# Optimization experiments

Measured on AMD Instinct MI355X. Metric: run time of the kernel, lower is better.

The kernel has to match this reference:

```python
import jax, jax.numpy as jnp
import numpy as np

N_NODES = 100000
N_EDGES = 1000000
HIDDEN = 64
IN_DIM = 4


def setup_inputs() -> dict:
    key = jax.random.key(0)
    ks = jax.random.split(key, 7)
    x = jax.random.normal(ks[0], (N_NODES, IN_DIM), dtype=jnp.float32)
    edges = jax.random.randint(ks[1], (N_EDGES, 2), 0, N_NODES, dtype=jnp.int32)
    W1 = jax.random.normal(ks[2], (IN_DIM, HIDDEN), dtype=jnp.float32) * 0.5
    b1 = jax.random.normal(ks[3], (HIDDEN,), dtype=jnp.float32) * 0.1
    phases = jax.random.normal(ks[4], (N_EDGES,), dtype=jnp.float32) * 0.1
    Wout = jax.random.normal(ks[5], (HIDDEN, 1), dtype=jnp.float32) * 0.1
    bout = jax.random.normal(ks[6], (1,), dtype=jnp.float32) * 0.1
    return {"x": x, "edges": edges, "W1": W1, "b1": b1,
            "phases": phases, "Wout": Wout, "bout": bout}


def reference(x, edges, W1, b1, phases, Wout, bout):
    # h = lin(x): [N, D]
    h = x @ W1 + b1
    u = edges[:, 0]  # [E]
    v = edges[:, 1]  # [E]
    c = jnp.cos(phases)  # [E]
    s = jnp.sin(phases)  # [E]
    hu = h[u]  # [E, D] gather
    hv = h[v]  # [E, D] gather
    # rot only mixes the first two channels; the rest pass through (eye).
    # msg to v: rot @ h[u] -> [c*h0 - s*h1, s*h0 + c*h1, h2, ...]
    msg_v = jnp.concatenate([
        (c * hu[:, 0] - s * hu[:, 1])[:, None],
        (s * hu[:, 0] + c * hu[:, 1])[:, None],
        hu[:, 2:],
    ], axis=1)
    # msg to u: rot.T @ h[v] -> [c*h0 + s*h1, -s*h0 + c*h1, h2, ...]
    msg_u = jnp.concatenate([
        (c * hv[:, 0] + s * hv[:, 1])[:, None],
        (-s * hv[:, 0] + c * hv[:, 1])[:, None],
        hv[:, 2:],
    ], axis=1)
    diffused = jnp.zeros_like(h).at[v].add(msg_v).at[u].add(msg_u)  # scatter-add
    return (h + diffused) @ Wout + bout  # [N, 1]
```

## Files before the change

kernel.cpp:

```cpp
#include <hip/hip_runtime.h>
#include <hip/hip_fp16.h>

#define N_NODES 100000
#define N_EDGES 1000000
#define HIDDEN 64

#define N_RANGES 3
#define C_RANGE 33344
#define N_SLICES 85
#define PAIRS (N_EDGES / 2)
#define PPB ((PAIRS + N_SLICES - 1) / N_SLICES)
#define A_THREADS 1024

__device__ __forceinline__ void compute_consts(
    const float* __restrict__ W1, const float* __restrict__ b1,
    const float* __restrict__ Wout, const float* __restrict__ bout,
    float* kc, int tid) {
    if (tid < 64) {
        float wj = Wout[tid];
        float p0 = W1[0 * HIDDEN + tid] * wj;
        float p1 = W1[1 * HIDDEN + tid] * wj;
        float p2 = W1[2 * HIDDEN + tid] * wj;
        float p3 = W1[3 * HIDDEN + tid] * wj;
        float pb = b1[tid] * wj;
        #pragma unroll
        for (int off = 32; off > 0; off >>= 1) {
            p0 += __shfl_down(p0, off);
            p1 += __shfl_down(p1, off);
            p2 += __shfl_down(p2, off);
            p3 += __shfl_down(p3, off);
            pb += __shfl_down(pb, off);
        }
        if (tid < 4) {
            kc[5 + tid] = W1[tid * HIDDEN + 0];
            kc[9 + tid] = W1[tid * HIDDEN + 1];
        }
        if (tid == 0) {
            kc[0] = p0; kc[1] = p1; kc[2] = p2; kc[3] = p3; kc[4] = pb;
            kc[13] = b1[0]; kc[14] = b1[1];
            kc[15] = Wout[0]; kc[16] = Wout[1];
            kc[17] = bout[0];
        }
    }
}

__device__ __forceinline__ float contrib(
    float4 xe, float cs, float sn_signed,
    float c0, float c1, float c2, float c3, float cb,
    float a0, float a1, float a2, float a3,
    float g0, float g1, float g2, float g3,
    float b10, float b11, float w0, float w1) {
    float h0 = xe.x * a0 + xe.y * a1 + xe.z * a2 + xe.w * a3 + b10;
    float h1 = xe.x * g0 + xe.y * g1 + xe.z * g2 + xe.w * g3 + b11;
    float d  = xe.x * c0 + xe.y * c1 + xe.z * c2 + xe.w * c3 + cb;
    float a  = h0 * w0 + h1 * w1;
    float b  = h0 * w1 - h1 * w0;
    return cs * a + sn_signed * b + (d - a);
}

__device__ __forceinline__ unsigned pack_half2(float x, float y) {
    __half2 h = __floats2half2_rn(x, y);
    return *(unsigned*)&h;
}

__global__ __launch_bounds__(A_THREADS) void range_kernel(
    const int2* __restrict__ edges, const float* __restrict__ phases,
    const float4* __restrict__ x4,
    const float* __restrict__ W1, const float* __restrict__ b1,
    const float* __restrict__ Wout, const float* __restrict__ bout,
    __half* __restrict__ part) {
    __shared__ float bins[C_RANGE];
    __shared__ float kc[18];
    const int tid = threadIdx.x;
    const int r = blockIdx.x / N_SLICES;
    const int s = blockIdx.x % N_SLICES;

    compute_consts(W1, b1, Wout, bout, kc, tid);
    {
        float4 z = make_float4(0.f, 0.f, 0.f, 0.f);
        float4* b4 = (float4*)bins;
        for (int j = tid; j < C_RANGE / 4; j += A_THREADS) b4[j] = z;
    }
    __syncthreads();

    const float c0 = kc[0], c1 = kc[1], c2 = kc[2], c3 = kc[3], cb = kc[4];
    const float a0 = kc[5], a1 = kc[6], a2 = kc[7], a3 = kc[8];
    const float g0 = kc[9], g1 = kc[10], g2 = kc[11], g3 = kc[12];
    const float b10 = kc[13], b11 = kc[14], w0 = kc[15], w1 = kc[16];

    const int nlo = r * C_RANGE;
    const int pA = s * PPB;
    const int pB = min(pA + PPB, PAIRS);
    const int4*   __restrict__ epairs = (const int4*)edges;
    const float2* __restrict__ ppairs = (const float2*)phases;

    #pragma unroll 2
    for (int p = pA + tid; p < pB; p += A_THREADS) {
        int4   ee = epairs[p];
        float2 pp = ppairs[p];

        unsigned jv0 = (unsigned)(ee.y - nlo);
        unsigned ju0 = (unsigned)(ee.x - nlo);
        unsigned jv1 = (unsigned)(ee.w - nlo);
        unsigned ju1 = (unsigned)(ee.z - nlo);
        bool pv0 = jv0 < C_RANGE, pu0 = ju0 < C_RANGE;
        bool pv1 = jv1 < C_RANGE, pu1 = ju1 < C_RANGE;

        float4 xsv0 = x4[pv0 ? ee.x : 0];
        float4 xsu0 = x4[pu0 ? ee.y : 0];
        float4 xsv1 = x4[pv1 ? ee.z : 0];
        float4 xsu1 = x4[pu1 ? ee.w : 0];

        float sn0, cs0, sn1, cs1;
        __sincosf(pp.x, &sn0, &cs0);
        __sincosf(pp.y, &sn1, &cs1);

        float tv0 = contrib(xsv0, cs0,  sn0, c0,c1,c2,c3,cb, a0,a1,a2,a3, g0,g1,g2,g3, b10,b11,w0,w1);
        float tu0 = contrib(xsu0, cs0, -sn0, c0,c1,c2,c3,cb, a0,a1,a2,a3, g0,g1,g2,g3, b10,b11,w0,w1);
        float tv1 = contrib(xsv1, cs1,  sn1, c0,c1,c2,c3,cb, a0,a1,a2,a3, g0,g1,g2,g3, b10,b11,w0,w1);
        float tu1 = contrib(xsu1, cs1, -sn1, c0,c1,c2,c3,cb, a0,a1,a2,a3, g0,g1,g2,g3, b10,b11,w0,w1);

        if (pv0) atomicAdd(&bins[jv0], tv0);
        if (pu0) atomicAdd(&bins[ju0], tu0);
        if (pv1) atomicAdd(&bins[jv1], tv1);
        if (pu1) atomicAdd(&bins[ju1], tu1);
    }
    __syncthreads();

    uint2* __restrict__ d2 = (uint2*)(part + (size_t)blockIdx.x * C_RANGE);
    const float4* b4 = (const float4*)bins;
    for (int j = tid; j < C_RANGE / 4; j += A_THREADS) {
        float4 v = b4[j];
        d2[j] = make_uint2(pack_half2(v.x, v.y), pack_half2(v.z, v.w));
    }
}

__global__ __launch_bounds__(512) void reduce_kernel(
    const float4* __restrict__ x4,
    const float* __restrict__ W1, const float* __restrict__ b1,
    const float* __restrict__ Wout, const float* __restrict__ bout,
    const __half* __restrict__ part, float* __restrict__ out) {
    __shared__ float kc[18];
    compute_consts(W1, b1, Wout, bout, kc, threadIdx.x);
    __syncthreads();
    int i = blockIdx.x * 512 + threadIdx.x;
    if (i >= N_NODES) return;
    int r = i / C_RANGE;
    int j = i - r * C_RANGE;
    const __half* __restrict__ p = part + ((size_t)(r * N_SLICES)) * C_RANGE + j;
    float sum = 0.0f;
    #pragma unroll 5
    for (int s = 0; s < N_SLICES; s++) sum += __half2float(p[(size_t)s * C_RANGE]);
    float4 xi = x4[i];
    out[i] = sum + xi.x * kc[0] + xi.y * kc[1] + xi.z * kc[2] + xi.w * kc[3]
           + kc[4] + kc[17];
}

__global__ void precompute_kernel(const float* __restrict__ W1,
                                  const float* __restrict__ b1,
                                  const float* __restrict__ Wout,
                                  const float* __restrict__ bout,
                                  float* __restrict__ consts) {
    __shared__ float kc[18];
    compute_consts(W1, b1, Wout, bout, kc, threadIdx.x);
    __syncthreads();
    if (threadIdx.x < 18) consts[threadIdx.x] = kc[threadIdx.x];
}

__global__ void edge_atomic_kernel(const int2* __restrict__ edges,
                                   const float* __restrict__ phases,
                                   const float4* __restrict__ x4,
                                   const float* __restrict__ consts,
                                   float* __restrict__ rep) {
    int e = blockIdx.x * blockDim.x + threadIdx.x;
    if (e >= N_EDGES) return;
    float c0 = consts[0], c1 = consts[1], c2 = consts[2], c3 = consts[3];
    float cb = consts[4];
    float a0 = consts[5], a1 = consts[6], a2 = consts[7], a3 = consts[8];
    float g0 = consts[9], g1 = consts[10], g2 = consts[11], g3 = consts[12];
    float b10 = consts[13], b11 = consts[14], w0 = consts[15], w1 = consts[16];
    int2 ed = edges[e];
    float ph = phases[e];
    float sn, cs;
    __sincosf(ph, &sn, &cs);
    float4 xu = x4[ed.x];
    float4 xv = x4[ed.y];
    atomicAdd(rep + ed.y, contrib(xu, cs,  sn, c0,c1,c2,c3,cb, a0,a1,a2,a3, g0,g1,g2,g3, b10,b11,w0,w1));
    atomicAdd(rep + ed.x, contrib(xv, cs, -sn, c0,c1,c2,c3,cb, a0,a1,a2,a3, g0,g1,g2,g3, b10,b11,w0,w1));
}

__global__ void final_kernel(const float4* __restrict__ x4,
                             const float* __restrict__ consts,
                             const float* __restrict__ rep,
                             float* __restrict__ out) {
    int i = blockIdx.x * blockDim.x + threadIdx.x;
    if (i >= N_NODES) return;
    float4 xi = x4[i];
    out[i] = rep[i] + xi.x * consts[0] + xi.y * consts[1] + xi.z * consts[2]
           + xi.w * consts[3] + consts[4] + consts[17];
}

extern "C" void kernel_launch(void* const* d_in, const int* in_sizes, int n_in,
                              void* d_out, int out_size, void* d_ws, size_t ws_size,
                              hipStream_t stream) {
    const float* x      = (const float*)d_in[0];
    const int*   edges  = (const int*)d_in[1];
    const float* W1     = (const float*)d_in[2];
    const float* b1     = (const float*)d_in[3];
    const float* phases = (const float*)d_in[4];
    const float* Wout   = (const float*)d_in[5];
    const float* bout   = (const float*)d_in[6];
    float* out = (float*)d_out;

    const size_t part_bytes =
        (size_t)N_RANGES * N_SLICES * C_RANGE * sizeof(__half);

    if (ws_size >= part_bytes) {
        __half* part = (__half*)d_ws;
        range_kernel<<<N_RANGES * N_SLICES, A_THREADS, 0, stream>>>(
            (const int2*)edges, phases, (const float4*)x,
            W1, b1, Wout, bout, part);
        reduce_kernel<<<(N_NODES + 511) / 512, 512, 0, stream>>>(
            (const float4*)x, W1, b1, Wout, bout, part, out);
    } else {
        float* consts = (float*)d_ws;
        float* rep    = (float*)((char*)d_ws + 256);
        hipMemsetAsync(rep, 0, N_NODES * sizeof(float), stream);
        precompute_kernel<<<1, 64, 0, stream>>>(W1, b1, Wout, bout, consts);
        edge_atomic_kernel<<<(N_EDGES + 255) / 256, 256, 0, stream>>>(
            (const int2*)edges, phases, (const float4*)x, consts, rep);
        final_kernel<<<(N_NODES + 255) / 256, 256, 0, stream>>>(
            (const float4*)x, consts, rep, out);
    }
}
```

Before: 98.78 us.

## Precompute per-node table, use two ranges with LDS bins plus global overflow atomics

Adds a prep kernel that computes a per-node float4 (a, b, d-a) once, so the edge kernel does two FMAs per message instead of recomputing the linear projection from x. Node ranges drop from 3 to 2 of 50000 nodes, each with 40704 LDS bins and 128 edge slices. Nodes that do not fit in LDS fall back to global atomics on an overflow array. This reads the edge list twice instead of three times and cuts per-edge ALU work, at the cost of global atomic traffic for the overflow nodes, an extra kernel launch and more partial-sum data to reduce.

```diff
diff --git a/kernel.cpp b/kernel.cpp
--- a/kernel.cpp
+++ b/kernel.cpp
@@ -5,9 +5,10 @@
 #define N_EDGES 1000000
 #define HIDDEN 64
 
-#define N_RANGES 3
-#define C_RANGE 33344
-#define N_SLICES 85
+#define N_RANGES 2
+#define R_SPAN   50000
+#define LDS_BINS 40704
+#define N_SLICES 128
 #define PAIRS (N_EDGES / 2)
 #define PPB ((PAIRS + N_SLICES - 1) / N_SLICES)
 #define A_THREADS 1024
@@ -63,36 +64,45 @@
     return *(unsigned*)&h;
 }
 
-__global__ __launch_bounds__(A_THREADS) void range_kernel(
-    const int2* __restrict__ edges, const float* __restrict__ phases,
+__global__ __launch_bounds__(512) void prep_kernel(
     const float4* __restrict__ x4,
     const float* __restrict__ W1, const float* __restrict__ b1,
     const float* __restrict__ Wout, const float* __restrict__ bout,
-    __half* __restrict__ part) {
-    __shared__ float bins[C_RANGE];
+    float4* __restrict__ tab, float* __restrict__ ov) {
     __shared__ float kc[18];
+    compute_consts(W1, b1, Wout, bout, kc, threadIdx.x);
+    __syncthreads();
+    int i = blockIdx.x * 512 + threadIdx.x;
+    if (i >= N_NODES) return;
+    float4 xi = x4[i];
+    float h0 = xi.x * kc[5] + xi.y * kc[6]  + xi.z * kc[7]  + xi.w * kc[8]  + kc[13];
+    float h1 = xi.x * kc[9] + xi.y * kc[10] + xi.z * kc[11] + xi.w * kc[12] + kc[14];
+    float d  = xi.x * kc[0] + xi.y * kc[1]  + xi.z * kc[2]  + xi.w * kc[3]  + kc[4];
+    float a  = h0 * kc[15] + h1 * kc[16];
+    float b  = h0 * kc[16] - h1 * kc[15];
+    tab[i] = make_float4(a, b, d - a, 0.f);
+    ov[i]  = 0.f;
+}
+
+__global__ __launch_bounds__(A_THREADS) void range_kernel(
+    const int4* __restrict__ epairs, const float2* __restrict__ ppairs,
+    const float4* __restrict__ tab,
+    float* __restrict__ ov, __half* __restrict__ part) {
+    __shared__ float bins[LDS_BINS];
     const int tid = threadIdx.x;
-    const int r = blockIdx.x / N_SLICES;
-    const int s = blockIdx.x % N_SLICES;
-
-    compute_consts(W1, b1, Wout, bout, kc, tid);
+    const int r = blockIdx.x >> 7;
+    const int s = blockIdx.x & 127;
+
     {
         float4 z = make_float4(0.f, 0.f, 0.f, 0.f);
         float4* b4 = (float4*)bins;
-        for (int j = tid; j < C_RANGE / 4; j += A_THREADS) b4[j] = z;
-    }
-    __syncthreads();
-
-    const float c0 = kc[0], c1 = kc[1], c2 = kc[2], c3 = kc[3], cb = kc[4];
-    const float a0 = kc[5], a1 = kc[6], a2 = kc[7], a3 = kc[8];
-    const float g0 = kc[9], g1 = kc[10], g2 = kc[11], g3 = kc[12];
-    const float b10 = kc[13], b11 = kc[14], w0 = kc[15], w1 = kc[16];
-
-    const int nlo = r * C_RANGE;
+        for (int j = tid; j < LDS_BINS / 4; j += A_THREADS) b4[j] = z;
+    }
+    __syncthreads();
+
+    const int nlo = r * R_SPAN;
     const int pA = s * PPB;
     const int pB = min(pA + PPB, PAIRS);
-    const int4*   __restrict__ epairs = (const int4*)edges;
-    const float2* __restrict__ ppairs = (const float2*)phases;
 
     #pragma unroll 2
     for (int p = pA + tid; p < pB; p += A_THREADS) {
@@ -103,33 +113,33 @@
         unsigned ju0 = (unsigned)(ee.x - nlo);
         unsigned jv1 = (unsigned)(ee.w - nlo);
         unsigned ju1 = (unsigned)(ee.z - nlo);
-        bool pv0 = jv0 < C_RANGE, pu0 = ju0 < C_RANGE;
-        bool pv1 = jv1 < C_RANGE, pu1 = ju1 < C_RANGE;
-
-        float4 xsv0 = x4[pv0 ? ee.x : 0];
-        float4 xsu0 = x4[pu0 ? ee.y : 0];
-        float4 xsv1 = x4[pv1 ? ee.z : 0];
-        float4 xsu1 = x4[pu1 ? ee.w : 0];
+        bool pv0 = jv0 < R_SPAN, pu0 = ju0 < R_SPAN;
+        bool pv1 = jv1 < R_SPAN, pu1 = ju1 < R_SPAN;
+
+        float4 tv0s = tab[pv0 ? ee.x : 0];
+        float4 tu0s = tab[pu0 ? ee.y : 0];
+        float4 tv1s = tab[pv1 ? ee.z : 0];
+        float4 tu1s = tab[pu1 ? ee.w : 0];
 
         float sn0, cs0, sn1, cs1;
         __sincosf(pp.x, &sn0, &cs0);
         __sincosf(pp.y, &sn1, &cs1);
 
-        float tv0 = contrib(xsv0, cs0,  sn0, c0,c1,c2,c3,cb, a0,a1,a2,a3, g0,g1,g2,g3, b10,b11,w0,w1);
-        float tu0 = contrib(xsu0, cs0, -sn0, c0,c1,c2,c3,cb, a0,a1,a2,a3, g0,g1,g2,g3, b10,b11,w0,w1);
-        float tv1 = contrib(xsv1, cs1,  sn1, c0,c1,c2,c3,cb, a0,a1,a2,a3, g0,g1,g2,g3, b10,b11,w0,w1);
-        float tu1 = contrib(xsu1, cs1, -sn1, c0,c1,c2,c3,cb, a0,a1,a2,a3, g0,g1,g2,g3, b10,b11,w0,w1);
-
-        if (pv0) atomicAdd(&bins[jv0], tv0);
-        if (pu0) atomicAdd(&bins[ju0], tu0);
-        if (pv1) atomicAdd(&bins[jv1], tv1);
-        if (pu1) atomicAdd(&bins[ju1], tu1);
-    }
-    __syncthreads();
-
-    uint2* __restrict__ d2 = (uint2*)(part + (size_t)blockIdx.x * C_RANGE);
+        float tv0 = fmaf(cs0, tv0s.x, fmaf( sn0, tv0s.y, tv0s.z));
+        float tu0 = fmaf(cs0, tu0s.x, fmaf(-sn0, tu0s.y, tu0s.z));
+        float tv1 = fmaf(cs1, tv1s.x, fmaf( sn1, tv1s.y, tv1s.z));
+        float tu1 = fmaf(cs1, tu1s.x, fmaf(-sn1, tu1s.y, tu1s.z));
+
+        if (pv0) { if (jv0 < LDS_BINS) atomicAdd(&bins[jv0], tv0); else atomicAdd(&ov[ee.y], tv0); }
+        if (pu0) { if (ju0 < LDS_BINS) atomicAdd(&bins[ju0], tu0); else atomicAdd(&ov[ee.x], tu0); }
+        if (pv1) { if (jv1 < LDS_BINS) atomicAdd(&bins[jv1], tv1); else atomicAdd(&ov[ee.w], tv1); }
+        if (pu1) { if (ju1 < LDS_BINS) atomicAdd(&bins[ju1], tu1); else atomicAdd(&ov[ee.z], tu1); }
+    }
+    __syncthreads();
+
+    uint2* __restrict__ d2 = (uint2*)(part + (size_t)blockIdx.x * LDS_BINS);
     const float4* b4 = (const float4*)bins;
-    for (int j = tid; j < C_RANGE / 4; j += A_THREADS) {
+    for (int j = tid; j < LDS_BINS / 4; j += A_THREADS) {
         float4 v = b4[j];
         d2[j] = make_uint2(pack_half2(v.x, v.y), pack_half2(v.z, v.w));
     }
@@ -139,18 +149,21 @@
     const float4* __restrict__ x4,
     const float* __restrict__ W1, const float* __restrict__ b1,
     const float* __restrict__ Wout, const float* __restrict__ bout,
-    const __half* __restrict__ part, float* __restrict__ out) {
+    const __half* __restrict__ part, const float* __restrict__ ov,
+    float* __restrict__ out) {
     __shared__ float kc[18];
     compute_consts(W1, b1, Wout, bout, kc, threadIdx.x);
     __syncthreads();
     int i = blockIdx.x * 512 + threadIdx.x;
     if (i >= N_NODES) return;
-    int r = i / C_RANGE;
-    int j = i - r * C_RANGE;
-    const __half* __restrict__ p = part + ((size_t)(r * N_SLICES)) * C_RANGE + j;
-    float sum = 0.0f;
-    #pragma unroll 5
-    for (int s = 0; s < N_SLICES; s++) sum += __half2float(p[(size_t)s * C_RANGE]);
+    int r = (i >= R_SPAN) ? 1 : 0;
+    int j = i - r * R_SPAN;
+    float sum = ov[i];
+    if (j < LDS_BINS) {
+        const __half* __restrict__ p = part + ((size_t)(r * N_SLICES)) * LDS_BINS + j;
+        #pragma unroll 8
+        for (int s = 0; s < N_SLICES; s++) sum += __half2float(p[(size_t)s * LDS_BINS]);
+    }
     float4 xi = x4[i];
     out[i] = sum + xi.x * kc[0] + xi.y * kc[1] + xi.z * kc[2] + xi.w * kc[3]
            + kc[4] + kc[17];
@@ -213,15 +226,23 @@
     float* out = (float*)d_out;
 
     const size_t part_bytes =
-        (size_t)N_RANGES * N_SLICES * C_RANGE * sizeof(__half);
-
-    if (ws_size >= part_bytes) {
+        (size_t)N_RANGES * N_SLICES * LDS_BINS * sizeof(__half);
+    const size_t tab_off  = part_bytes;
+    const size_t tab_bytes = (size_t)N_NODES * sizeof(float4);
+    const size_t ov_off   = tab_off + tab_bytes;
+    const size_t ov_bytes = (size_t)N_NODES * sizeof(float);
+    const size_t need     = ov_off + ov_bytes;
+
+    if (ws_size >= need) {
         __half* part = (__half*)d_ws;
+        float4* tab  = (float4*)((char*)d_ws + tab_off);
+        float*  ov   = (float*)((char*)d_ws + ov_off);
+        prep_kernel<<<(N_NODES + 511) / 512, 512, 0, stream>>>(
+            (const float4*)x, W1, b1, Wout, bout, tab, ov);
         range_kernel<<<N_RANGES * N_SLICES, A_THREADS, 0, stream>>>(
-            (const int2*)edges, phases, (const float4*)x,
-            W1, b1, Wout, bout, part);
+            (const int4*)edges, (const float2*)phases, tab, ov, part);
         reduce_kernel<<<(N_NODES + 511) / 512, 512, 0, stream>>>(
-            (const float4*)x, W1, b1, Wout, bout, part, out);
+            (const float4*)x, W1, b1, Wout, bout, part, ov, out);
     } else {
         float* consts = (float*)d_ws;
         float* rep    = (float*)((char*)d_ws + 256);
```

New measurement: 123.4 us. +25.0%, slower.

## Precompute per-node projection table and vectorize reduce to half2 pairs

Applied to the files above, without the earlier changes.

Adds a prep kernel that computes, for each node, the projected terms (a, b, d-a) once and stores them in a float4 table. The range kernel now gathers from this table and needs only two FMAs per endpoint instead of recomputing the linear projection on every edge. The reduce kernel now handles two nodes per thread, reading half2 partials and writing float2 outputs. The cost is an extra kernel launch and a 1.6MB table write and read, and the gather volume per edge is unchanged.

```diff
diff --git a/kernel.cpp b/kernel.cpp
--- a/kernel.cpp
+++ b/kernel.cpp
@@ -63,19 +63,33 @@
     return *(unsigned*)&h;
 }
 
-__global__ __launch_bounds__(A_THREADS) void range_kernel(
-    const int2* __restrict__ edges, const float* __restrict__ phases,
+__global__ __launch_bounds__(512) void prep_kernel(
     const float4* __restrict__ x4,
     const float* __restrict__ W1, const float* __restrict__ b1,
     const float* __restrict__ Wout, const float* __restrict__ bout,
-    __half* __restrict__ part) {
+    float4* __restrict__ tab) {
+    __shared__ float kc[18];
+    compute_consts(W1, b1, Wout, bout, kc, threadIdx.x);
+    __syncthreads();
+    int i = blockIdx.x * 512 + threadIdx.x;
+    if (i >= N_NODES) return;
+    float4 xi = x4[i];
+    float h0 = xi.x * kc[5] + xi.y * kc[6]  + xi.z * kc[7]  + xi.w * kc[8]  + kc[13];
+    float h1 = xi.x * kc[9] + xi.y * kc[10] + xi.z * kc[11] + xi.w * kc[12] + kc[14];
+    float d  = xi.x * kc[0] + xi.y * kc[1]  + xi.z * kc[2]  + xi.w * kc[3]  + kc[4];
+    float a  = h0 * kc[15] + h1 * kc[16];
+    float b  = h0 * kc[16] - h1 * kc[15];
+    tab[i] = make_float4(a, b, d - a, 0.f);
+}
+
+__global__ __launch_bounds__(A_THREADS) void range_kernel(
+    const int4* __restrict__ epairs, const float2* __restrict__ ppairs,
+    const float4* __restrict__ tab, __half* __restrict__ part) {
     __shared__ float bins[C_RANGE];
-    __shared__ float kc[18];
     const int tid = threadIdx.x;
     const int r = blockIdx.x / N_SLICES;
-    const int s = blockIdx.x % N_SLICES;
-
-    compute_consts(W1, b1, Wout, bout, kc, tid);
+    const int s = blockIdx.x - r * N_SLICES;
+
     {
         float4 z = make_float4(0.f, 0.f, 0.f, 0.f);
         float4* b4 = (float4*)bins;
@@ -83,16 +97,9 @@
     }
     __syncthreads();
 
-    const float c0 = kc[0], c1 = kc[1], c2 = kc[2], c3 = kc[3], cb = kc[4];
-    const float a0 = kc[5], a1 = kc[6], a2 = kc[7], a3 = kc[8];
-    const float g0 = kc[9], g1 = kc[10], g2 = kc[11], g3 = kc[12];
-    const float b10 = kc[13], b11 = kc[14], w0 = kc[15], w1 = kc[16];
-
     const int nlo = r * C_RANGE;
     const int pA = s * PPB;
     const int pB = min(pA + PPB, PAIRS);
-    const int4*   __restrict__ epairs = (const int4*)edges;
-    const float2* __restrict__ ppairs = (const float2*)phases;
 
     #pragma unroll 2
     for (int p = pA + tid; p < pB; p += A_THREADS) {
@@ -106,19 +113,19 @@
         bool pv0 = jv0 < C_RANGE, pu0 = ju0 < C_RANGE;
         bool pv1 = jv1 < C_RANGE, pu1 = ju1 < C_RANGE;
 
-        float4 xsv0 = x4[pv0 ? ee.x : 0];
-        float4 xsu0 = x4[pu0 ? ee.y : 0];
-        float4 xsv1 = x4[pv1 ? ee.z : 0];
-        float4 xsu1 = x4[pu1 ? ee.w : 0];
+        float4 tv0s = tab[pv0 ? ee.x : 0];
+        float4 tu0s = tab[pu0 ? ee.y : 0];
+        float4 tv1s = tab[pv1 ? ee.z : 0];
+        float4 tu1s = tab[pu1 ? ee.w : 0];
 
         float sn0, cs0, sn1, cs1;
         __sincosf(pp.x, &sn0, &cs0);
         __sincosf(pp.y, &sn1, &cs1);
 
-        float tv0 = contrib(xsv0, cs0,  sn0, c0,c1,c2,c3,cb, a0,a1,a2,a3, g0,g1,g2,g3, b10,b11,w0,w1);
-        float tu0 = contrib(xsu0, cs0, -sn0, c0,c1,c2,c3,cb, a0,a1,a2,a3, g0,g1,g2,g3, b10,b11,w0,w1);
-        float tv1 = contrib(xsv1, cs1,  sn1, c0,c1,c2,c3,cb, a0,a1,a2,a3, g0,g1,g2,g3, b10,b11,w0,w1);
-        float tu1 = contrib(xsu1, cs1, -sn1, c0,c1,c2,c3,cb, a0,a1,a2,a3, g0,g1,g2,g3, b10,b11,w0,w1);
+        float tv0 = fmaf(cs0, tv0s.x, fmaf( sn0, tv0s.y, tv0s.z));
+        float tu0 = fmaf(cs0, tu0s.x, fmaf(-sn0, tu0s.y, tu0s.z));
+        float tv1 = fmaf(cs1, tv1s.x, fmaf( sn1, tv1s.y, tv1s.z));
+        float tu1 = fmaf(cs1, tu1s.x, fmaf(-sn1, tu1s.y, tu1s.z));
 
         if (pv0) atomicAdd(&bins[jv0], tv0);
         if (pu0) atomicAdd(&bins[ju0], tu0);
@@ -139,21 +146,29 @@
     const float4* __restrict__ x4,
     const float* __restrict__ W1, const float* __restrict__ b1,
     const float* __restrict__ Wout, const float* __restrict__ bout,
-    const __half* __restrict__ part, float* __restrict__ out) {
+    const __half2* __restrict__ part2, float2* __restrict__ out2) {
     __shared__ float kc[18];
     compute_consts(W1, b1, Wout, bout, kc, threadIdx.x);
     __syncthreads();
-    int i = blockIdx.x * 512 + threadIdx.x;
-    if (i >= N_NODES) return;
-    int r = i / C_RANGE;
-    int j = i - r * C_RANGE;
-    const __half* __restrict__ p = part + ((size_t)(r * N_SLICES)) * C_RANGE + j;
-    float sum = 0.0f;
+    int t = blockIdx.x * 512 + threadIdx.x;
+    int i0 = t * 2;
+    if (i0 >= N_NODES) return;
+    int r = i0 / C_RANGE;
+    int j = i0 - r * C_RANGE;
+    const __half2* __restrict__ p = part2
+        + (size_t)(r * N_SLICES) * (C_RANGE / 2) + (j >> 1);
+    float s0 = 0.0f, s1 = 0.0f;
     #pragma unroll 5
-    for (int s = 0; s < N_SLICES; s++) sum += __half2float(p[(size_t)s * C_RANGE]);
-    float4 xi = x4[i];
-    out[i] = sum + xi.x * kc[0] + xi.y * kc[1] + xi.z * kc[2] + xi.w * kc[3]
-           + kc[4] + kc[17];
+    for (int s = 0; s < N_SLICES; s++) {
+        float2 v = __half22float2(p[(size_t)s * (C_RANGE / 2)]);
+        s0 += v.x; s1 += v.y;
+    }
+    float4 xa = x4[i0];
+    float4 xb = x4[i0 + 1];
+    float base = kc[4] + kc[17];
+    out2[t] = make_float2(
+        s0 + xa.x * kc[0] + xa.y * kc[1] + xa.z * kc[2] + xa.w * kc[3] + base,
+        s1 + xb.x * kc[0] + xb.y * kc[1] + xb.z * kc[2] + xb.w * kc[3] + base);
 }
 
 __global__ void precompute_kernel(const float* __restrict__ W1,
@@ -214,14 +229,20 @@
 
     const size_t part_bytes =
         (size_t)N_RANGES * N_SLICES * C_RANGE * sizeof(__half);
-
-    if (ws_size >= part_bytes) {
+    const size_t tab_off   = part_bytes;
+    const size_t tab_bytes = (size_t)N_NODES * sizeof(float4);
+    const size_t need      = tab_off + tab_bytes;
+
+    if (ws_size >= need) {
         __half* part = (__half*)d_ws;
+        float4* tab  = (float4*)((char*)d_ws + tab_off);
+        prep_kernel<<<(N_NODES + 511) / 512, 512, 0, stream>>>(
+            (const float4*)x, W1, b1, Wout, bout, tab);
         range_kernel<<<N_RANGES * N_SLICES, A_THREADS, 0, stream>>>(
-            (const int2*)edges, phases, (const float4*)x,
-            W1, b1, Wout, bout, part);
-        reduce_kernel<<<(N_NODES + 511) / 512, 512, 0, stream>>>(
-            (const float4*)x, W1, b1, Wout, bout, part, out);
+            (const int4*)edges, (const float2*)phases, tab, part);
+        reduce_kernel<<<(N_NODES / 2 + 511) / 512, 512, 0, stream>>>(
+            (const float4*)x, W1, b1, Wout, bout,
+            (const __half2*)part, (float2*)out);
     } else {
         float* consts = (float*)d_ws;
         float* rep    = (float*)((char*)d_ws + 256);
```

Result: slower. 101.4 us (+2.7%).

## Fuse range and reduce kernels via cooperative launch with grid sync

Applied to the files above, without the earlier changes.

Merges the binning kernel and the slice-reduction kernel into one cooperative kernel separated by a grid-wide barrier, falling back to the two-kernel path if the cooperative launch fails. The goal is to remove the second kernel launch and the inter-kernel gap. In exchange it requires all 255 blocks of 1024 threads with about 133KB of LDS each to be co-resident, and the grid sync adds its own cost. The reduction runs on 1024-thread blocks in place of 512.

```diff
diff --git a/kernel.cpp b/kernel.cpp
--- a/kernel.cpp
+++ b/kernel.cpp
@@ -1,5 +1,8 @@
 #include <hip/hip_runtime.h>
 #include <hip/hip_fp16.h>
+#include <hip/hip_cooperative_groups.h>
+
+namespace cg = cooperative_groups;
 
 #define N_NODES 100000
 #define N_EDGES 1000000
@@ -63,25 +66,13 @@
     return *(unsigned*)&h;
 }
 
-__global__ __launch_bounds__(A_THREADS) void range_kernel(
-    const int2* __restrict__ edges, const float* __restrict__ phases,
-    const float4* __restrict__ x4,
-    const float* __restrict__ W1, const float* __restrict__ b1,
-    const float* __restrict__ Wout, const float* __restrict__ bout,
-    __half* __restrict__ part) {
-    __shared__ float bins[C_RANGE];
-    __shared__ float kc[18];
-    const int tid = threadIdx.x;
-    const int r = blockIdx.x / N_SLICES;
-    const int s = blockIdx.x % N_SLICES;
-
-    compute_consts(W1, b1, Wout, bout, kc, tid);
-    {
-        float4 z = make_float4(0.f, 0.f, 0.f, 0.f);
-        float4* b4 = (float4*)bins;
-        for (int j = tid; j < C_RANGE / 4; j += A_THREADS) b4[j] = z;
-    }
-    __syncthreads();
+__device__ __forceinline__ void do_range(
+    const int4* __restrict__ epairs, const float2* __restrict__ ppairs,
+    const float4* __restrict__ x4, const float* __restrict__ kc,
+    float* __restrict__ bins, __half* __restrict__ part,
+    int blockId, int tid) {
+    const int r = blockId / N_SLICES;
+    const int s = blockId - r * N_SLICES;
 
     const float c0 = kc[0], c1 = kc[1], c2 = kc[2], c3 = kc[3], cb = kc[4];
     const float a0 = kc[5], a1 = kc[6], a2 = kc[7], a3 = kc[8];
@@ -91,8 +82,6 @@
     const int nlo = r * C_RANGE;
     const int pA = s * PPB;
     const int pB = min(pA + PPB, PAIRS);
-    const int4*   __restrict__ epairs = (const int4*)edges;
-    const float2* __restrict__ ppairs = (const float2*)phases;
 
     #pragma unroll 2
     for (int p = pA + tid; p < pB; p += A_THREADS) {
@@ -127,7 +116,7 @@
     }
     __syncthreads();
 
-    uint2* __restrict__ d2 = (uint2*)(part + (size_t)blockIdx.x * C_RANGE);
+    uint2* __restrict__ d2 = (uint2*)(part + (size_t)blockId * C_RANGE);
     const float4* b4 = (const float4*)bins;
     for (int j = tid; j < C_RANGE / 4; j += A_THREADS) {
         float4 v = b4[j];
@@ -135,6 +124,61 @@
     }
 }
 
+__global__ __launch_bounds__(A_THREADS) void fused_kernel(
+    const int4* __restrict__ epairs, const float2* __restrict__ ppairs,
+    const float4* __restrict__ x4,
+    const float* __restrict__ W1, const float* __restrict__ b1,
+    const float* __restrict__ Wout, const float* __restrict__ bout,
+    __half* __restrict__ part, float* __restrict__ out) {
+    __shared__ __align__(16) float bins[C_RANGE];
+    __shared__ float kc[18];
+    const int tid = threadIdx.x;
+
+    compute_consts(W1, b1, Wout, bout, kc, tid);
+    {
+        float4 z = make_float4(0.f, 0.f, 0.f, 0.f);
+        float4* b4 = (float4*)bins;
+        for (int j = tid; j < C_RANGE / 4; j += A_THREADS) b4[j] = z;
+    }
+    __syncthreads();
+
+    do_range(epairs, ppairs, x4, kc, bins, part, blockIdx.x, tid);
+
+    cg::this_grid().sync();
+
+    int i = blockIdx.x * A_THREADS + tid;
+    if (i < N_NODES) {
+        int r = i / C_RANGE;
+        int j = i - r * C_RANGE;
+        const __half* __restrict__ p = part + (size_t)(r * N_SLICES) * C_RANGE + j;
+        float sum = 0.0f;
+        #pragma unroll 5
+        for (int s = 0; s < N_SLICES; s++) sum += __half2float(p[(size_t)s * C_RANGE]);
+        float4 xi = x4[i];
+        out[i] = sum + xi.x * kc[0] + xi.y * kc[1] + xi.z * kc[2] + xi.w * kc[3]
+               + kc[4] + kc[17];
+    }
+}
+
+__global__ __launch_bounds__(A_THREADS) void range_kernel(
+    const int4* __restrict__ epairs, const float2* __restrict__ ppairs,
+    const float4* __restrict__ x4,
+    const float* __restrict__ W1, const float* __restrict__ b1,
+    const float* __restrict__ Wout, const float* __restrict__ bout,
+    __half* __restrict__ part) {
+    __shared__ __align__(16) float bins[C_RANGE];
+    __shared__ float kc[18];
+    const int tid = threadIdx.x;
+    compute_consts(W1, b1, Wout, bout, kc, tid);
+    {
+        float4 z = make_float4(0.f, 0.f, 0.f, 0.f);
+        float4* b4 = (float4*)bins;
+        for (int j = tid; j < C_RANGE / 4; j += A_THREADS) b4[j] = z;
+    }
+    __syncthreads();
+    do_range(epairs, ppairs, x4, kc, bins, part, blockIdx.x, tid);
+}
+
 __global__ __launch_bounds__(512) void reduce_kernel(
     const float4* __restrict__ x4,
     const float* __restrict__ W1, const float* __restrict__ b1,
@@ -147,7 +191,7 @@
     if (i >= N_NODES) return;
     int r = i / C_RANGE;
     int j = i - r * C_RANGE;
-    const __half* __restrict__ p = part + ((size_t)(r * N_SLICES)) * C_RANGE + j;
+    const __half* __restrict__ p = part + (size_t)(r * N_SLICES) * C_RANGE + j;
     float sum = 0.0f;
     #pragma unroll 5
     for (int s = 0; s < N_SLICES; s++) sum += __half2float(p[(size_t)s * C_RANGE]);
@@ -217,11 +261,25 @@
 
     if (ws_size >= part_bytes) {
         __half* part = (__half*)d_ws;
-        range_kernel<<<N_RANGES * N_SLICES, A_THREADS, 0, stream>>>(
-            (const int2*)edges, phases, (const float4*)x,
-            W1, b1, Wout, bout, part);
-        reduce_kernel<<<(N_NODES + 511) / 512, 512, 0, stream>>>(
-            (const float4*)x, W1, b1, Wout, bout, part, out);
+        const int4*   epairs = (const int4*)edges;
+        const float2* ppairs = (const float2*)phases;
+        const float4* x4     = (const float4*)x;
+
+        void* args[] = {
+            (void*)&epairs, (void*)&ppairs, (void*)&x4,
+            (void*)&W1, (void*)&b1, (void*)&Wout, (void*)&bout,
+            (void*)&part, (void*)&out };
+        hipError_t err = hipLaunchCooperativeKernel(
+            (const void*)fused_kernel,
+            dim3(N_RANGES * N_SLICES), dim3(A_THREADS),
+            args, 0, stream);
+        if (err != hipSuccess) {
+            (void)hipGetLastError();
+            range_kernel<<<N_RANGES * N_SLICES, A_THREADS, 0, stream>>>(
+                epairs, ppairs, x4, W1, b1, Wout, bout, part);
+            reduce_kernel<<<(N_NODES + 511) / 512, 512, 0, stream>>>(
+                x4, W1, b1, Wout, bout, part, out);
+        }
     } else {
         float* consts = (float*)d_ws;
         float* rep    = (float*)((char*)d_ws + 256);
```

Result: slower. 155.3 us (+57.2%).
